# Kernel optimization log

Hardware: AMD Instinct MI355X
Metric: run time of the kernel (lower is better)

The kernel has to match this reference:

```python
import jax, jax.numpy as jnp
import numpy as np

B, S, D, H, DFF = 4, 2048, 1024, 16, 4096
HD = D // H


def setup_inputs() -> dict:
    key = jax.random.key(0)
    ks = jax.random.split(key, 12)
    sc = 0.02
    return {
        "x": jax.random.normal(ks[0], (B, S, D), jnp.float32),
        "wq": jax.random.normal(ks[1], (HD, HD), jnp.float32) * sc,
        "bq": jnp.zeros((HD,), jnp.float32),
        "wk": jax.random.normal(ks[2], (HD, HD), jnp.float32) * sc,
        "bk": jnp.zeros((HD,), jnp.float32),
        "wv": jax.random.normal(ks[3], (HD, HD), jnp.float32) * sc,
        "bv": jnp.zeros((HD,), jnp.float32),
        "wo": jax.random.normal(ks[4], (D, D), jnp.float32) * sc,
        "bo": jnp.zeros((D,), jnp.float32),
        "ln1_w": jnp.ones((D,), jnp.float32),
        "ln1_b": jnp.zeros((D,), jnp.float32),
        "w1": jax.random.normal(ks[5], (D, DFF), jnp.float32) * sc,
        "b1": jnp.zeros((DFF,), jnp.float32),
        "w2": jax.random.normal(ks[6], (DFF, D), jnp.float32) * sc,
        "b2": jnp.zeros((D,), jnp.float32),
        "ln2_w": jnp.ones((D,), jnp.float32),
        "ln2_b": jnp.zeros((D,), jnp.float32),
    }


def _layernorm(x, w, b, eps=1e-5):
    m = jnp.mean(x, axis=-1, keepdims=True)
    v = jnp.mean((x - m) ** 2, axis=-1, keepdims=True)
    return (x - m) / jnp.sqrt(v + eps) * w + b


def reference(x, wq, bq, wk, bk, wv, bv, wo, bo, ln1_w, ln1_b, w1, b1, w2, b2, ln2_w, ln2_b):
    bs, s, d = x.shape
    h = H
    hd = d // h
    # split heads: [b, h, s, hd]
    xh = x.reshape(bs, s, h, hd).transpose(0, 2, 1, 3)
    q = xh @ wq + bq  # per-head-dim linear, shared across heads (as in source)
    k = xh @ wk + bk
    v = xh @ wv + bv
    scores = jnp.einsum("bhqd,bhkd->bhqk", q, k) / (hd ** 0.5)
    # faithful quirk: tril then mask-where-zero -> -inf
    tri = jnp.tril(scores)
    masked = jnp.where(tri == 0, -jnp.inf, tri)
    attn = jax.nn.softmax(masked, axis=-1)
    o = attn @ v  # [b, h, s, hd]
    o = o.transpose(0, 2, 1, 3).reshape(bs, s, d)
    o = o @ wo + bo
    x = _layernorm(x + o, ln1_w, ln1_b)
    ff = jax.nn.gelu(x @ w1 + b1, approximate=False) @ w2 + b2  # dropout is identity in eval
    x = _layernorm(x + ff, ln2_w, ln2_b)
    return x
```

## Files before the change

### kernel.cpp

```cpp
#include <hip/hip_runtime.h>

typedef unsigned short u16;
typedef unsigned int u32;
typedef float f32x4 __attribute__((ext_vector_type(4)));
typedef short s16x8 __attribute__((ext_vector_type(8)));
typedef u16 u16x8 __attribute__((ext_vector_type(8)));
typedef u32 u32x4 __attribute__((ext_vector_type(4)));

#define DEV static __device__ __forceinline__

DEV u16 f2bf(float f){
  unsigned u = __float_as_uint(f);
  u += 0x7fffu + ((u>>16)&1u);
  return (u16)(u>>16);
}

DEV float bf2f(u16 h){ return __uint_as_float((u32)h << 16); }

DEV u32 cvt_pk_bf16(float lo, float hi){
  u32 r;
  asm("v_cvt_pk_bf16_f32 %0, %1, %2" : "=v"(r) : "v"(lo), "v"(hi));
  return r;
}

DEV f32x4 mfma_bf16(s16x8 a, s16x8 b, f32x4 c){
  return __builtin_amdgcn_mfma_f32_16x16x32_bf16(a, b, c, 0, 0, 0);
}

DEV void gll16(const void* g, void* l){
  __builtin_amdgcn_global_load_lds((const __attribute__((address_space(1))) u32*)g,
                                   (__attribute__((address_space(3))) u32*)l, 16, 0, 0);
}

__global__ __launch_bounds__(256) void transpose_cast(const float* __restrict__ w,
                                                      u16* __restrict__ wt,
                                                      int K, int N){
  __shared__ float tile[32][33];
  int n0 = blockIdx.x * 32, k0 = blockIdx.y * 32;
  int tx = threadIdx.x & 31, ty = threadIdx.x >> 5;
  #pragma unroll
  for(int j = 0; j < 32; j += 8)
    tile[ty + j][tx] = w[(size_t)(k0 + ty + j) * N + n0 + tx];
  __syncthreads();
  #pragma unroll
  for(int j = 0; j < 32; j += 8)
    wt[(size_t)(n0 + ty + j) * K + k0 + tx] = f2bf(tile[tx][ty + j]);
}

__global__ __launch_bounds__(256) void qkv_kernel(const float* __restrict__ x,
    const float* __restrict__ wq, const float* __restrict__ bq,
    const float* __restrict__ wk, const float* __restrict__ bk,
    const float* __restrict__ wv, const float* __restrict__ bv,
    u16* __restrict__ qo, u16* __restrict__ ko, u16* __restrict__ vo){
  __shared__ float ws[3 * 64 * 64];
  __shared__ float xs[32 * 64];
  __shared__ float vls[64 * 33];
  int h  = blockIdx.y;
  int r0 = blockIdx.x * 32;
  for(int i = threadIdx.x; i < 1024; i += 256) ((float4*)ws)[i]        = ((const float4*)wq)[i];
  for(int i = threadIdx.x; i < 1024; i += 256) ((float4*)ws)[1024 + i] = ((const float4*)wk)[i];
  for(int i = threadIdx.x; i < 1024; i += 256) ((float4*)ws)[2048 + i] = ((const float4*)wv)[i];
  for(int i = threadIdx.x; i < 512; i += 256){
    int r = i >> 4, c4 = (i & 15) * 4;
    ((float4*)xs)[i] = *(const float4*)(x + (size_t)(r0 + r) * 1024 + h * 64 + c4);
  }
  __syncthreads();
  int r  = threadIdx.x >> 3;
  int j0 = (threadIdx.x & 7) * 8;
  float aq[8], ak[8], av[8];
  #pragma unroll
  for(int j = 0; j < 8; j++){ aq[j] = 0.f; ak[j] = 0.f; av[j] = 0.f; }
  for(int i = 0; i < 64; i++){
    float xv = xs[r * 64 + i];
    const float* wr = ws + i * 64 + j0;
    #pragma unroll
    for(int j = 0; j < 8; j++){
      aq[j] = fmaf(xv, wr[j],        aq[j]);
      ak[j] = fmaf(xv, wr[4096 + j], ak[j]);
      av[j] = fmaf(xv, wr[8192 + j], av[j]);
    }
  }
  int b = r0 >> 11, s0 = r0 & 2047;
  int bh = b * 16 + h;
  size_t base = ((size_t)bh * 2048 + s0 + r) * 64 + j0;
  ushort4 q_lo = { f2bf(aq[0]+bq[j0+0]), f2bf(aq[1]+bq[j0+1]), f2bf(aq[2]+bq[j0+2]), f2bf(aq[3]+bq[j0+3]) };
  ushort4 q_hi = { f2bf(aq[4]+bq[j0+4]), f2bf(aq[5]+bq[j0+5]), f2bf(aq[6]+bq[j0+6]), f2bf(aq[7]+bq[j0+7]) };
  ushort4 k_lo = { f2bf(ak[0]+bk[j0+0]), f2bf(ak[1]+bk[j0+1]), f2bf(ak[2]+bk[j0+2]), f2bf(ak[3]+bk[j0+3]) };
  ushort4 k_hi = { f2bf(ak[4]+bk[j0+4]), f2bf(ak[5]+bk[j0+5]), f2bf(ak[6]+bk[j0+6]), f2bf(ak[7]+bk[j0+7]) };
  *(ushort4*)(qo + base)     = q_lo;  *(ushort4*)(qo + base + 4) = q_hi;
  *(ushort4*)(ko + base)     = k_lo;  *(ushort4*)(ko + base + 4) = k_hi;
  #pragma unroll
  for(int j = 0; j < 8; j++) vls[(j0 + j) * 33 + r] = av[j] + bv[j0 + j];
  __syncthreads();
  size_t vtb = (size_t)bh * 64 * 2048 + s0;
  for(int i = threadIdx.x; i < 2048; i += 256){
    int d = i >> 5, sl = i & 31;
    vo[vtb + (size_t)d * 2048 + sl] = f2bf(vls[d * 33 + sl]);
  }
}

__global__ __launch_bounds__(256, 5) void attn_kernel(const u16* __restrict__ q,
                                                      const u16* __restrict__ k,
                                                      const u16* __restrict__ vT,
                                                      u16* __restrict__ o){
  __shared__ u16 ksh[2 * 64 * 64];
  __shared__ u16 vsh[2 * 64 * 64];
  int bi = blockIdx.x;
  int bh = bi & 63;
  int qt = 31 - (bi >> 6);
  int w = threadIdx.x >> 6, lane = threadIdx.x & 63;
  int l15 = lane & 15, l4 = lane >> 4;
  size_t kvbase = (size_t)bh * 2048 * 64;
  size_t vtbase = (size_t)bh * 64 * 2048;
  int b_ = bh >> 4, h = bh & 15;
  f32x4 zero = {0.f, 0.f, 0.f, 0.f};

  int r8 = lane >> 3, c8 = lane & 7;
  int swz = ((c8 ^ r8) << 3);
  int roff = (l15 & 7) << 3;
  int rx   = l15 & 7;
  int o4   = (l4 & 1) << 2;

  s16x8 qf[2];
  #pragma unroll
  for(int kc = 0; kc < 2; kc++){
    u16x8 qr = *(const u16x8*)(q + kvbase + (size_t)(qt*64 + w*16 + l15)*64 + kc*32 + l4*8);
    union { u32x4 u; s16x8 h; } pk;
    #pragma unroll
    for(int r = 0; r < 4; r++)
      pk.u[r] = cvt_pk_bf16(bf2f(qr[2*r]) * 0.125f, bf2f(qr[2*r+1]) * 0.125f);
    qf[kc] = pk.h;
  }

  f32x4 accO[4];
  #pragma unroll
  for(int md = 0; md < 4; md++) accO[md] = zero;
  float lrow = 0.f;

  #pragma unroll
  for(int j = 0; j < 2; j++){
    int row = w*16 + j*8 + r8;
    gll16(k  + kvbase + (size_t)row*64 + swz,   ksh + row*64 + c8*8);
    gll16(vT + vtbase + (size_t)row*2048 + swz, vsh + row*64 + c8*8);
  }
  __syncthreads();

  #pragma unroll 1
  for(int kt = 0; kt <= qt; kt++){
    int cur = kt & 1;
    if(kt < qt){
      int nb = cur ^ 1, k1 = kt + 1;
      #pragma unroll
      for(int j = 0; j < 2; j++){
        int row = w*16 + j*8 + r8;
        gll16(k  + kvbase + (size_t)(k1*64 + row)*64 + swz,  ksh + nb*4096 + row*64 + c8*8);
        gll16(vT + vtbase + (size_t)row*2048 + k1*64 + swz,  vsh + nb*4096 + row*64 + c8*8);
      }
    }
    const u16* kb = ksh + cur*4096;
    const u16* vb = vsh + cur*4096;

    f32x4 sc[4];
    #pragma unroll
    for(int mk = 0; mk < 4; mk++){
      s16x8 kf0 = *(const s16x8*)(kb + (mk*16 + l15)*64 + ((l4*8) ^ roff));
      s16x8 kf1 = *(const s16x8*)(kb + (mk*16 + l15)*64 + ((32 + l4*8) ^ roff));
      f32x4 a = zero;
      a = mfma_bf16(kf0, qf[0], a);
      a = mfma_bf16(kf1, qf[1], a);
      sc[mk] = a;
    }
    if(kt == qt){
      int ql = w*16 + l15;
      #pragma unroll
      for(int mk = 0; mk < 4; mk++){
        int kl = mk*16 + l4*4;
        #pragma unroll
        for(int b = 0; b < 4; b++)
          if(kl + b > ql) sc[mk][b] = -3.0e38f;
      }
    }
    #pragma unroll
    for(int mk = 0; mk < 4; mk++)
      #pragma unroll
      for(int b = 0; b < 4; b++)
        sc[mk][b] = __expf(fminf(sc[mk][b], 8.f));
    f32x4 s4 = sc[0] + sc[1] + sc[2] + sc[3];
    lrow += (s4[0] + s4[1]) + (s4[2] + s4[3]);

    u32 plo[4], phi[4];
    #pragma unroll
    for(int mk = 0; mk < 4; mk++){
      plo[mk] = cvt_pk_bf16(sc[mk][0], sc[mk][1]);
      phi[mk] = cvt_pk_bf16(sc[mk][2], sc[mk][3]);
    }
    #pragma unroll
    for(int kc = 0; kc < 2; kc++){
      union { u32x4 u; s16x8 h; } pb;
      pb.u[0] = plo[2*kc];   pb.u[1] = phi[2*kc];
      pb.u[2] = plo[2*kc+1]; pb.u[3] = phi[2*kc+1];
      int bB = 4*kc + (l4 >> 1);
      s16x8 vf[4];
      #pragma unroll
      for(int md = 0; md < 4; md++){
        const u16* vrow = vb + (md*16 + l15)*64;
        union { struct{ uint2 a, b; } p; s16x8 h; } vv;
        vv.p.a = *(const uint2*)(vrow + (((bB    ) ^ rx) << 3) + o4);
        vv.p.b = *(const uint2*)(vrow + (((bB + 2) ^ rx) << 3) + o4);
        vf[md] = vv.h;
      }
      __builtin_amdgcn_s_setprio(1);
      #pragma unroll
      for(int md = 0; md < 4; md++)
        accO[md] = mfma_bf16(vf[md], pb.h, accO[md]);
      __builtin_amdgcn_s_setprio(0);
    }
    __syncthreads();
  }

  lrow += __shfl_xor(lrow, 16);
  lrow += __shfl_xor(lrow, 32);
  float inv = 1.f / lrow;
  int qrow = qt*64 + w*16 + l15;
  #pragma unroll
  for(int md = 0; md < 4; md++){
    int d0 = md*16 + l4*4;
    ushort4 ov;
    ov.x = f2bf(accO[md][0] * inv);
    ov.y = f2bf(accO[md][1] * inv);
    ov.z = f2bf(accO[md][2] * inv);
    ov.w = f2bf(accO[md][3] * inv);
    *(ushort4*)(o + ((size_t)(b_*2048 + qrow))*1024 + h*64 + d0) = ov;
  }
}

template<int EPI, int BM, int BN, int WM, int WN>
__global__ __launch_bounds__(WM*WN*64) void gemm_dbuf(const u16* __restrict__ A,
    const u16* __restrict__ Bt, const float* __restrict__ bias,
    const float* __restrict__ resid, float* __restrict__ Cf,
    int M, int N, int K, int ntn){
  constexpr int THREADS = WM*WN*64;
  constexpr int RM = BM/(WM*16), RN = BN/(WN*16);
  constexpr int LDSH = (BM+BN)*64;
  constexpr int RSTEP = THREADS/8;
  constexpr int PA = BM/RSTEP, PB = BN/RSTEP;
  __shared__ u16 lds[2*LDSH];

  int nwg = gridDim.x;
  int cq = nwg >> 3;
  int wg = ((int)blockIdx.x & 7) * cq + ((int)blockIdx.x >> 3);
  int tm = wg / ntn, tn = wg % ntn;

  int tid = threadIdx.x, lane = tid & 63, w = tid >> 6;
  int wm = w / WN, wn = w % WN;
  int l15 = lane & 15, l4 = lane >> 4;

  f32x4 zero = {0.f, 0.f, 0.f, 0.f};
  f32x4 acc[RM][RN];
  #pragma unroll
  for(int m = 0; m < RM; m++)
    #pragma unroll
    for(int n = 0; n < RN; n++) acc[m][n] = zero;

  int srow = tid >> 3, scol = (tid & 7) * 8;
  const u16* Ag = A  + ((size_t)tm*BM + srow)*(size_t)K + scol;
  const u16* Bg = Bt + ((size_t)tn*BN + srow)*(size_t)K + scol;
  int ldsAo = srow*64 + scol;
  int ldsBo = BM*64 + srow*64 + scol;

  int NT = K >> 6;
  #pragma unroll
  for(int p = 0; p < PA; p++) gll16(Ag + (size_t)p*RSTEP*K, lds + ldsAo + p*RSTEP*64);
  #pragma unroll
  for(int p = 0; p < PB; p++) gll16(Bg + (size_t)p*RSTEP*K, lds + ldsBo + p*RSTEP*64);
  __syncthreads();

  int wr = wm * (BM/WM), wc = wn * (BN/WN);
  for(int t = 0; t < NT; t++){
    const u16* buf = lds + (t & 1) * LDSH;
    if(t + 1 < NT){
      u16* nbuf = lds + ((t + 1) & 1) * LDSH;
      int kt = (t + 1) << 6;
      #pragma unroll
      for(int p = 0; p < PA; p++) gll16(Ag + (size_t)p*RSTEP*K + kt, nbuf + ldsAo + p*RSTEP*64);
      #pragma unroll
      for(int p = 0; p < PB; p++) gll16(Bg + (size_t)p*RSTEP*K + kt, nbuf + ldsBo + p*RSTEP*64);
    }
    #pragma unroll
    for(int kc = 0; kc < 2; kc++){
      s16x8 af[RM], bfr[RN];
      #pragma unroll
      for(int m = 0; m < RM; m++) af[m]  = *(const s16x8*)(buf + (wr + m*16 + l15)*64 + kc*32 + l4*8);
      #pragma unroll
      for(int n = 0; n < RN; n++) bfr[n] = *(const s16x8*)(buf + BM*64 + (wc + n*16 + l15)*64 + kc*32 + l4*8);
      #pragma unroll
      for(int m = 0; m < RM; m++)
        #pragma unroll
        for(int n = 0; n < RN; n++)
          acc[m][n] = mfma_bf16(af[m], bfr[n], acc[m][n]);
    }
    __syncthreads();
  }

  int row0 = tm*BM + wr, col0 = tn*BN + wc;
  #pragma unroll
  for(int n = 0; n < RN; n++){
    int col = col0 + n*16 + l15;
    float bcol = bias[col];
    #pragma unroll
    for(int m = 0; m < RM; m++){
      #pragma unroll
      for(int b4 = 0; b4 < 4; b4++){
        int row = row0 + m*16 + l4*4 + b4;
        size_t oi = (size_t)row * N + col;
        Cf[oi] = acc[m][n][b4] + bcol + resid[oi];
      }
    }
  }
}

template<int EPI, int BN, int SPLITK>
__global__ __launch_bounds__(512, 2) void gemm_8ph(const u16* __restrict__ A,
    const u16* __restrict__ Bt, const float* __restrict__ bias,
    float* __restrict__ Cf, u16* __restrict__ Cb,
    int M, int N, int LDA, int Kloop, int ntn){
  constexpr int NPP = BN / 128;
  constexpr int BLOADS = BN / 128;
  __shared__ u16 lds[32768 + 4 * BN * 32];

  auto Aoff = [](int b, int kc){ return b*16384 + kc*8192; };
  auto Boff = [](int b, int kc){ return 32768 + (b*2 + kc) * BN * 32; };

  int nwg = gridDim.x;
  int cq = nwg >> 3;
  int wg = ((int)blockIdx.x & 7) * cq + ((int)blockIdx.x >> 3);
  int ks = 0;
  if constexpr (SPLITK == 2){ ks = wg & 1; wg >>= 1; }
  int tm = wg / ntn, tn = wg % ntn;

  int tid = threadIdx.x, lane = tid & 63, w = tid >> 6;
  int wm = w >> 2, wn = w & 3;
  int l15 = lane & 15, l4 = lane >> 4;

  const u16* Ag = A  + (size_t)tm * 256 * LDA + (size_t)ks * Kloop;
  const u16* Bg = Bt + (size_t)tn * BN  * LDA + (size_t)ks * Kloop;

  f32x4 zero = {0.f, 0.f, 0.f, 0.f};
  f32x4 acc[8][2*NPP];
  #pragma unroll
  for(int m = 0; m < 8; m++)
    #pragma unroll
    for(int n = 0; n < 2*NPP; n++) acc[m][n] = zero;

  int NT = Kloop >> 6;

  auto stA = [&](int st, int skc, int sbuf){
    #pragma unroll
    for(int j = 0; j < 2; j++){
      int row = (tid >> 2) + j * 128;
      int sc = (((tid & 3) ^ ((row >> 1) & 3)) << 3);
      gll16(Ag + (size_t)row * LDA + st*64 + skc*32 + sc,
            lds + Aoff(sbuf, skc) + row*32 + (tid & 3)*8);
    }
  };
  auto stB = [&](int st, int skc, int sbuf){
    #pragma unroll
    for(int j = 0; j < BLOADS; j++){
      int row = (tid >> 2) + j * 128;
      int sc = (((tid & 3) ^ ((row >> 1) & 3)) << 3);
      gll16(Bg + (size_t)row * LDA + st*64 + skc*32 + sc,
            lds + Boff(sbuf, skc) + row*32 + (tid & 3)*8);
    }
  };

  stA(0, 0, 0); stB(0, 0, 0);
  stA(0, 1, 0); stB(0, 1, 0);
  stA(1, 0, 1); stB(1, 0, 1);
  stA(1, 1, 1);
  if constexpr (BN == 256) asm volatile("s_waitcnt vmcnt(4)" ::: "memory");
  else                     asm volatile("s_waitcnt vmcnt(3)" ::: "memory");
  __builtin_amdgcn_s_barrier();

  s16x8 af[8], bf[NPP];
  for(int it = 0; it < (NT >> 1); ++it){
    int t0 = it << 1;
    #pragma unroll
    for(int p = 0; p < 8; p++){
      const int nh = p & 1, kc = (p >> 1) & 1, bsel = p >> 2;
      if(nh == 0){
        #pragma unroll
        for(int m = 0; m < 8; m++){
          int arow = wm*128 + m*16 + l15;
          af[m] = *(const s16x8*)(lds + Aoff(bsel, kc) + arow*32 + ((l4 ^ ((arow>>1)&3)) << 3));
        }
      }
      #pragma unroll
      for(int n = 0; n < NPP; n++){
        int brow = wn*(BN/4) + nh*(BN/8) + n*16 + l15;
        bf[n] = *(const s16x8*)(lds + Boff(bsel, kc) + brow*32 + ((l4 ^ ((brow>>1)&3)) << 3));
      }
      {
        constexpr int SKC[8] = {1,0,0,1,1,0,0,1};
        constexpr int SBF[8] = {1,0,0,0,0,1,1,1};
        constexpr int TOF[8] = {1,2,2,2,2,3,3,3};
        int st = t0 + TOF[p]; if(st > NT - 1) st = NT - 1;
        if(p & 1) stA(st, SKC[p], SBF[p]);
        else      stB(st, SKC[p], SBF[p]);
      }
      __builtin_amdgcn_s_barrier();
      asm volatile("s_waitcnt lgkmcnt(0)" ::: "memory");
      __builtin_amdgcn_s_setprio(1);
      #pragma unroll
      for(int m = 0; m < 8; m++)
        #pragma unroll
        for(int n = 0; n < NPP; n++)
          acc[m][nh*NPP + n] = mfma_bf16(af[m], bf[n], acc[m][nh*NPP + n]);
      __builtin_amdgcn_s_setprio(0);
      if(p == 3 || p == 7){
        if constexpr (BN == 256) asm volatile("s_waitcnt vmcnt(4)" ::: "memory");
        else                     asm volatile("s_waitcnt vmcnt(3)" ::: "memory");
      }
      __builtin_amdgcn_s_barrier();
    }
  }

  int row0 = tm*256 + wm*128, col0 = tn*BN + wn*(BN/4);
  float* Cfp = Cf;
  if constexpr (EPI == 3) Cfp = Cf + (size_t)ks * M * N;
  #pragma unroll
  for(int nh = 0; nh < 2; nh++)
    #pragma unroll
    for(int n = 0; n < NPP; n++){
      int j = nh*NPP + n;
      int col = col0 + nh*(BN/8) + n*16 + l15;
      float bcol = 0.f;
      if constexpr (EPI == 1) bcol = bias[col];
      #pragma unroll
      for(int m = 0; m < 8; m++){
        #pragma unroll
        for(int b4 = 0; b4 < 4; b4++){
          int row = row0 + m*16 + l4*4 + b4;
          size_t oi = (size_t)row * N + col;
          if constexpr (EPI == 1){
            float vout = acc[m][j][b4] + bcol;
            float uu = 0.7978845608f * vout * (1.f + 0.044715f * vout * vout);
            float e  = __expf(2.f * uu);
            float th = 1.f - __fdividef(2.f, e + 1.f);
            Cb[oi] = f2bf(0.5f * vout * (1.f + th));
          } else {
            Cfp[oi] = acc[m][j][b4];
          }
        }
      }
    }
}

__global__ __launch_bounds__(256) void ln_kernel(const float* __restrict__ a,
                                                 const float* __restrict__ w,
                                                 const float* __restrict__ bvec,
                                                 u16* __restrict__ outb){
  int row = blockIdx.x;
  float4 val = ((const float4*)(a + (size_t)row * 1024))[threadIdx.x];
  float s  = val.x + val.y + val.z + val.w;
  float ss = val.x * val.x + val.y * val.y + val.z * val.z + val.w * val.w;
  #pragma unroll
  for(int off = 32; off > 0; off >>= 1){
    s  += __shfl_down(s, off);
    ss += __shfl_down(ss, off);
  }
  __shared__ float sb[8];
  int lane = threadIdx.x & 63, wv = threadIdx.x >> 6;
  if(lane == 0){ sb[wv] = s; sb[4 + wv] = ss; }
  __syncthreads();
  s  = sb[0] + sb[1] + sb[2] + sb[3];
  ss = sb[4] + sb[5] + sb[6] + sb[7];
  float mean = s * (1.f / 1024.f);
  float var  = ss * (1.f / 1024.f) - mean * mean;
  float rstd = rsqrtf(var + 1e-5f);
  int c = threadIdx.x * 4;
  float4 w4 = *(const float4*)(w + c);
  float4 b4 = *(const float4*)(bvec + c);
  ushort4 ob;
  ob.x = f2bf((val.x - mean) * rstd * w4.x + b4.x);
  ob.y = f2bf((val.y - mean) * rstd * w4.y + b4.y);
  ob.z = f2bf((val.z - mean) * rstd * w4.z + b4.z);
  ob.w = f2bf((val.w - mean) * rstd * w4.w + b4.w);
  *(ushort4*)(outb + (size_t)row * 1024 + c) = ob;
}

__global__ __launch_bounds__(256) void ln2_kernel(const float* __restrict__ p0,
                                                  const float* __restrict__ p1,
                                                  const u16* __restrict__ residb,
                                                  const float* __restrict__ b2,
                                                  const float* __restrict__ w,
                                                  const float* __restrict__ bvec,
                                                  float* __restrict__ outf){
  int row = blockIdx.x;
  int c = threadIdx.x * 4;
  float4 v0 = ((const float4*)(p0 + (size_t)row * 1024))[threadIdx.x];
  float4 v1 = ((const float4*)(p1 + (size_t)row * 1024))[threadIdx.x];
  ushort4 rb = *(const ushort4*)(residb + (size_t)row * 1024 + c);
  float4 bb = *(const float4*)(b2 + c);
  float4 val;
  val.x = v0.x + v1.x + bb.x + bf2f(rb.x);
  val.y = v0.y + v1.y + bb.y + bf2f(rb.y);
  val.z = v0.z + v1.z + bb.z + bf2f(rb.z);
  val.w = v0.w + v1.w + bb.w + bf2f(rb.w);
  float s  = val.x + val.y + val.z + val.w;
  float ss = val.x * val.x + val.y * val.y + val.z * val.z + val.w * val.w;
  #pragma unroll
  for(int off = 32; off > 0; off >>= 1){
    s  += __shfl_down(s, off);
    ss += __shfl_down(ss, off);
  }
  __shared__ float sb[8];
  int lane = threadIdx.x & 63, wv = threadIdx.x >> 6;
  if(lane == 0){ sb[wv] = s; sb[4 + wv] = ss; }
  __syncthreads();
  s  = sb[0] + sb[1] + sb[2] + sb[3];
  ss = sb[4] + sb[5] + sb[6] + sb[7];
  float mean = s * (1.f / 1024.f);
  float var  = ss * (1.f / 1024.f) - mean * mean;
  float rstd = rsqrtf(var + 1e-5f);
  float4 w4 = *(const float4*)(w + c);
  float4 b4 = *(const float4*)(bvec + c);
  float4 o4v;
  o4v.x = (val.x - mean) * rstd * w4.x + b4.x;
  o4v.y = (val.y - mean) * rstd * w4.y + b4.y;
  o4v.z = (val.z - mean) * rstd * w4.z + b4.z;
  o4v.w = (val.w - mean) * rstd * w4.w + b4.w;
  ((float4*)(outf + (size_t)row * 1024))[threadIdx.x] = o4v;
}

extern "C" void kernel_launch(void* const* d_in, const int* in_sizes, int n_in,
                              void* d_out, int out_size, void* d_ws, size_t ws_size,
                              hipStream_t stream){
  const float* x    = (const float*)d_in[0];
  const float* wq   = (const float*)d_in[1];
  const float* bq   = (const float*)d_in[2];
  const float* wk   = (const float*)d_in[3];
  const float* bk   = (const float*)d_in[4];
  const float* wv   = (const float*)d_in[5];
  const float* bv   = (const float*)d_in[6];
  const float* wo   = (const float*)d_in[7];
  const float* bo   = (const float*)d_in[8];
  const float* ln1w = (const float*)d_in[9];
  const float* ln1b = (const float*)d_in[10];
  const float* w1   = (const float*)d_in[11];
  const float* b1   = (const float*)d_in[12];
  const float* w2   = (const float*)d_in[13];
  const float* b2   = (const float*)d_in[14];
  const float* ln2w = (const float*)d_in[15];
  const float* ln2b = (const float*)d_in[16];
  float* out = (float*)d_out;

  char* ws8 = (char*)d_ws;
  u16*   qb  = (u16*)  (ws8 + ((size_t)0   << 20));
  u16*   kb  = (u16*)  (ws8 + ((size_t)16  << 20));
  u16*   vb  = (u16*)  (ws8 + ((size_t)32  << 20));
  u16*   ob  = (u16*)  (ws8 + ((size_t)48  << 20));
  u16*   wot = (u16*)  (ws8 + ((size_t)64  << 20));
  u16*   w1t = (u16*)  (ws8 + ((size_t)66  << 20));
  u16*   w2t = (u16*)  (ws8 + ((size_t)74  << 20));
  u16*   tb  = (u16*)  (ws8 + ((size_t)82  << 20));
  u16*   gb  = (u16*)  (ws8 + ((size_t)98  << 20));
  float* rr  = (float*)(ws8 + ((size_t)162 << 20));

  transpose_cast<<<dim3(32, 32),  256, 0, stream>>>(wo, wot, 1024, 1024);
  transpose_cast<<<dim3(128, 32), 256, 0, stream>>>(w1, w1t, 1024, 4096);
  transpose_cast<<<dim3(32, 128), 256, 0, stream>>>(w2, w2t, 4096, 1024);

  qkv_kernel<<<dim3(256, 16), 256, 0, stream>>>(x, wq, bq, wk, bk, wv, bv, qb, kb, vb);
  attn_kernel<<<dim3(2048), 256, 0, stream>>>(qb, kb, vb, ob);

  gemm_dbuf<0,128,128,2,2><<<dim3(512), 256, 0, stream>>>(ob, wot, bo, x, rr, 8192, 1024, 1024, 8);
  ln_kernel<<<dim3(8192), 256, 0, stream>>>(rr, ln1w, ln1b, tb);
  gemm_8ph<1,256,1><<<dim3(512), 512, 0, stream>>>(tb, w1t, b1, nullptr, gb, 8192, 4096, 1024, 1024, 16);
  gemm_8ph<3,256,2><<<dim3(256), 512, 0, stream>>>(gb, w2t, nullptr, rr, nullptr, 8192, 1024, 4096, 2048, 4);
  ln2_kernel<<<dim3(8192), 256, 0, stream>>>(rr, rr + (size_t)8192*1024, tb, b2, ln2w, ln2b, out);
}
```

Baseline: 385.5 us.

## Process two N-tiles per workgroup in FFN1 GEMM and store split-K partials as bf16

The FFN1 GEMM now has each workgroup compute two adjacent 256-wide N tiles in sequence, reusing the A tile's address setup. The next tile's prologue loads are issued before the epilogue of the current one, and the grid is halved to 256 workgroups. The split-K FFN2 GEMM now writes its partial sums as bf16 instead of fp32, and ln2 reads them as bf16, which halves the partial-sum traffic. Fewer workgroups means less parallelism per CU wave, and rounding the partials to bf16 reduces accuracy.

```diff
diff --git a/kernel.cpp b/kernel.cpp
--- a/kernel.cpp
+++ b/kernel.cpp
@@ -319,7 +319,7 @@
   }
 }
 
-template<int EPI, int BN, int SPLITK>
+template<int EPI, int BN, int SPLITK, int PAIR>
 __global__ __launch_bounds__(512, 2) void gemm_8ph(const u16* __restrict__ A,
     const u16* __restrict__ Bt, const float* __restrict__ bias,
     float* __restrict__ Cf, u16* __restrict__ Cb,
@@ -336,21 +336,13 @@
   int wg = ((int)blockIdx.x & 7) * cq + ((int)blockIdx.x >> 3);
   int ks = 0;
   if constexpr (SPLITK == 2){ ks = wg & 1; wg >>= 1; }
-  int tm = wg / ntn, tn = wg % ntn;
+  int tm = wg / ntn, tnp = wg % ntn;
 
   int tid = threadIdx.x, lane = tid & 63, w = tid >> 6;
   int wm = w >> 2, wn = w & 3;
   int l15 = lane & 15, l4 = lane >> 4;
 
-  const u16* Ag = A  + (size_t)tm * 256 * LDA + (size_t)ks * Kloop;
-  const u16* Bg = Bt + (size_t)tn * BN  * LDA + (size_t)ks * Kloop;
-
-  f32x4 zero = {0.f, 0.f, 0.f, 0.f};
-  f32x4 acc[8][2*NPP];
-  #pragma unroll
-  for(int m = 0; m < 8; m++)
-    #pragma unroll
-    for(int n = 0; n < 2*NPP; n++) acc[m][n] = zero;
+  const u16* Ag = A + (size_t)tm * 256 * LDA + (size_t)ks * Kloop;
 
   int NT = Kloop >> 6;
 
@@ -363,7 +355,7 @@
             lds + Aoff(sbuf, skc) + row*32 + (tid & 3)*8);
     }
   };
-  auto stB = [&](int st, int skc, int sbuf){
+  auto stB = [&](const u16* Bg, int st, int skc, int sbuf){
     #pragma unroll
     for(int j = 0; j < BLOADS; j++){
       int row = (tid >> 2) + j * 128;
@@ -372,87 +364,115 @@
             lds + Boff(sbuf, skc) + row*32 + (tid & 3)*8);
     }
   };
-
-  stA(0, 0, 0); stB(0, 0, 0);
-  stA(0, 1, 0); stB(0, 1, 0);
-  stA(1, 0, 1); stB(1, 0, 1);
-  stA(1, 1, 1);
-  if constexpr (BN == 256) asm volatile("s_waitcnt vmcnt(4)" ::: "memory");
-  else                     asm volatile("s_waitcnt vmcnt(3)" ::: "memory");
-  __builtin_amdgcn_s_barrier();
-
+  auto prologue = [&](const u16* Bg){
+    stA(0, 0, 0); stB(Bg, 0, 0, 0);
+    stA(0, 1, 0); stB(Bg, 0, 1, 0);
+    stA(1, 0, 1); stB(Bg, 1, 0, 1);
+    stA(1, 1, 1);
+  };
+
+  f32x4 zero = {0.f, 0.f, 0.f, 0.f};
+  f32x4 acc[8][2*NPP];
   s16x8 af[8], bf[NPP];
-  for(int it = 0; it < (NT >> 1); ++it){
-    int t0 = it << 1;
-    #pragma unroll
-    for(int p = 0; p < 8; p++){
-      const int nh = p & 1, kc = (p >> 1) & 1, bsel = p >> 2;
-      if(nh == 0){
+
+  #pragma unroll
+  for(int sub = 0; sub < PAIR; ++sub){
+    int tn = tnp * PAIR + sub;
+    const u16* Bg = Bt + (size_t)tn * BN * LDA + (size_t)ks * Kloop;
+    #pragma unroll
+    for(int m = 0; m < 8; m++)
+      #pragma unroll
+      for(int n = 0; n < 2*NPP; n++) acc[m][n] = zero;
+
+    if(sub == 0){
+      prologue(Bg);
+      if constexpr (BN == 256) asm volatile("s_waitcnt vmcnt(4)" ::: "memory");
+      else                     asm volatile("s_waitcnt vmcnt(3)" ::: "memory");
+      __builtin_amdgcn_s_barrier();
+    }
+
+    for(int it = 0; it < (NT >> 1); ++it){
+      int t0 = it << 1;
+      #pragma unroll
+      for(int p = 0; p < 8; p++){
+        const int nh = p & 1, kc = (p >> 1) & 1, bsel = p >> 2;
+        if(nh == 0){
+          #pragma unroll
+          for(int m = 0; m < 8; m++){
+            int arow = wm*128 + m*16 + l15;
+            af[m] = *(const s16x8*)(lds + Aoff(bsel, kc) + arow*32 + ((l4 ^ ((arow>>1)&3)) << 3));
+          }
+        }
+        #pragma unroll
+        for(int n = 0; n < NPP; n++){
+          int brow = wn*(BN/4) + nh*(BN/8) + n*16 + l15;
+          bf[n] = *(const s16x8*)(lds + Boff(bsel, kc) + brow*32 + ((l4 ^ ((brow>>1)&3)) << 3));
+        }
+        {
+          constexpr int SKC[8] = {1,0,0,1,1,0,0,1};
+          constexpr int SBF[8] = {1,0,0,0,0,1,1,1};
+          constexpr int TOF[8] = {1,2,2,2,2,3,3,3};
+          int st = t0 + TOF[p]; if(st > NT - 1) st = NT - 1;
+          if(p & 1) stA(st, SKC[p], SBF[p]);
+          else      stB(Bg, st, SKC[p], SBF[p]);
+        }
+        __builtin_amdgcn_s_barrier();
+        asm volatile("s_waitcnt lgkmcnt(0)" ::: "memory");
+        __builtin_amdgcn_s_setprio(1);
+        #pragma unroll
+        for(int m = 0; m < 8; m++)
+          #pragma unroll
+          for(int n = 0; n < NPP; n++)
+            acc[m][nh*NPP + n] = mfma_bf16(af[m], bf[n], acc[m][nh*NPP + n]);
+        __builtin_amdgcn_s_setprio(0);
+        if(p == 3 || p == 7){
+          if constexpr (BN == 256) asm volatile("s_waitcnt vmcnt(4)" ::: "memory");
+          else                     asm volatile("s_waitcnt vmcnt(3)" ::: "memory");
+        }
+        __builtin_amdgcn_s_barrier();
+      }
+    }
+
+    if(sub + 1 < PAIR){
+      asm volatile("s_waitcnt vmcnt(0)" ::: "memory");
+      const u16* Bg2 = Bt + (size_t)(tn + 1) * BN * LDA + (size_t)ks * Kloop;
+      prologue(Bg2);
+    }
+
+    int row0 = tm*256 + wm*128, col0 = tn*BN + wn*(BN/4);
+    #pragma unroll
+    for(int nh = 0; nh < 2; nh++)
+      #pragma unroll
+      for(int n = 0; n < NPP; n++){
+        int j = nh*NPP + n;
+        int col = col0 + nh*(BN/8) + n*16 + l15;
+        float bcol = 0.f;
+        if constexpr (EPI == 1) bcol = bias[col];
         #pragma unroll
         for(int m = 0; m < 8; m++){
-          int arow = wm*128 + m*16 + l15;
-          af[m] = *(const s16x8*)(lds + Aoff(bsel, kc) + arow*32 + ((l4 ^ ((arow>>1)&3)) << 3));
-        }
-      }
-      #pragma unroll
-      for(int n = 0; n < NPP; n++){
-        int brow = wn*(BN/4) + nh*(BN/8) + n*16 + l15;
-        bf[n] = *(const s16x8*)(lds + Boff(bsel, kc) + brow*32 + ((l4 ^ ((brow>>1)&3)) << 3));
-      }
-      {
-        constexpr int SKC[8] = {1,0,0,1,1,0,0,1};
-        constexpr int SBF[8] = {1,0,0,0,0,1,1,1};
-        constexpr int TOF[8] = {1,2,2,2,2,3,3,3};
-        int st = t0 + TOF[p]; if(st > NT - 1) st = NT - 1;
-        if(p & 1) stA(st, SKC[p], SBF[p]);
-        else      stB(st, SKC[p], SBF[p]);
-      }
-      __builtin_amdgcn_s_barrier();
-      asm volatile("s_waitcnt lgkmcnt(0)" ::: "memory");
-      __builtin_amdgcn_s_setprio(1);
-      #pragma unroll
-      for(int m = 0; m < 8; m++)
-        #pragma unroll
-        for(int n = 0; n < NPP; n++)
-          acc[m][nh*NPP + n] = mfma_bf16(af[m], bf[n], acc[m][nh*NPP + n]);
-      __builtin_amdgcn_s_setprio(0);
-      if(p == 3 || p == 7){
-        if constexpr (BN == 256) asm volatile("s_waitcnt vmcnt(4)" ::: "memory");
-        else                     asm volatile("s_waitcnt vmcnt(3)" ::: "memory");
-      }
-      __builtin_amdgcn_s_barrier();
-    }
-  }
-
-  int row0 = tm*256 + wm*128, col0 = tn*BN + wn*(BN/4);
-  float* Cfp = Cf;
-  if constexpr (EPI == 3) Cfp = Cf + (size_t)ks * M * N;
-  #pragma unroll
-  for(int nh = 0; nh < 2; nh++)
-    #pragma unroll
-    for(int n = 0; n < NPP; n++){
-      int j = nh*NPP + n;
-      int col = col0 + nh*(BN/8) + n*16 + l15;
-      float bcol = 0.f;
-      if constexpr (EPI == 1) bcol = bias[col];
-      #pragma unroll
-      for(int m = 0; m < 8; m++){
-        #pragma unroll
-        for(int b4 = 0; b4 < 4; b4++){
-          int row = row0 + m*16 + l4*4 + b4;
-          size_t oi = (size_t)row * N + col;
-          if constexpr (EPI == 1){
-            float vout = acc[m][j][b4] + bcol;
-            float uu = 0.7978845608f * vout * (1.f + 0.044715f * vout * vout);
-            float e  = __expf(2.f * uu);
-            float th = 1.f - __fdividef(2.f, e + 1.f);
-            Cb[oi] = f2bf(0.5f * vout * (1.f + th));
-          } else {
-            Cfp[oi] = acc[m][j][b4];
+          #pragma unroll
+          for(int b4 = 0; b4 < 4; b4++){
+            int row = row0 + m*16 + l4*4 + b4;
+            size_t oi = (size_t)row * N + col;
+            if constexpr (EPI == 1){
+              float vout = acc[m][j][b4] + bcol;
+              float uu = 0.7978845608f * vout * (1.f + 0.044715f * vout * vout);
+              float e  = __expf(2.f * uu);
+              float th = 1.f - __fdividef(2.f, e + 1.f);
+              Cb[oi] = f2bf(0.5f * vout * (1.f + th));
+            } else {
+              Cb[(size_t)ks * M * N + oi] = f2bf(acc[m][j][b4]);
+            }
           }
         }
       }
-    }
+
+    if(sub + 1 < PAIR){
+      if constexpr (BN == 256) asm volatile("s_waitcnt vmcnt(4)" ::: "memory");
+      else                     asm volatile("s_waitcnt vmcnt(3)" ::: "memory");
+      __builtin_amdgcn_s_barrier();
+    }
+  }
 }
 
 __global__ __launch_bounds__(256) void ln_kernel(const float* __restrict__ a,
@@ -488,8 +508,8 @@
   *(ushort4*)(outb + (size_t)row * 1024 + c) = ob;
 }
 
-__global__ __launch_bounds__(256) void ln2_kernel(const float* __restrict__ p0,
-                                                  const float* __restrict__ p1,
+__global__ __launch_bounds__(256) void ln2_kernel(const u16* __restrict__ p0,
+                                                  const u16* __restrict__ p1,
                                                   const u16* __restrict__ residb,
                                                   const float* __restrict__ b2,
                                                   const float* __restrict__ w,
@@ -497,15 +517,15 @@
                                                   float* __restrict__ outf){
   int row = blockIdx.x;
   int c = threadIdx.x * 4;
-  float4 v0 = ((const float4*)(p0 + (size_t)row * 1024))[threadIdx.x];
-  float4 v1 = ((const float4*)(p1 + (size_t)row * 1024))[threadIdx.x];
+  ushort4 v0 = *(const ushort4*)(p0 + (size_t)row * 1024 + c);
+  ushort4 v1 = *(const ushort4*)(p1 + (size_t)row * 1024 + c);
   ushort4 rb = *(const ushort4*)(residb + (size_t)row * 1024 + c);
   float4 bb = *(const float4*)(b2 + c);
   float4 val;
-  val.x = v0.x + v1.x + bb.x + bf2f(rb.x);
-  val.y = v0.y + v1.y + bb.y + bf2f(rb.y);
-  val.z = v0.z + v1.z + bb.z + bf2f(rb.z);
-  val.w = v0.w + v1.w + bb.w + bf2f(rb.w);
+  val.x = bf2f(v0.x) + bf2f(v1.x) + bb.x + bf2f(rb.x);
+  val.y = bf2f(v0.y) + bf2f(v1.y) + bb.y + bf2f(rb.y);
+  val.z = bf2f(v0.z) + bf2f(v1.z) + bb.z + bf2f(rb.z);
+  val.w = bf2f(v0.w) + bf2f(v1.w) + bb.w + bf2f(rb.w);
   float s  = val.x + val.y + val.z + val.w;
   float ss = val.x * val.x + val.y * val.y + val.z * val.z + val.w * val.w;
   #pragma unroll
@@ -565,6 +585,7 @@
   u16*   tb  = (u16*)  (ws8 + ((size_t)82  << 20));
   u16*   gb  = (u16*)  (ws8 + ((size_t)98  << 20));
   float* rr  = (float*)(ws8 + ((size_t)162 << 20));
+  u16*   pp  = (u16*)  (ws8 + ((size_t)162 << 20));
 
   transpose_cast<<<dim3(32, 32),  256, 0, stream>>>(wo, wot, 1024, 1024);
   transpose_cast<<<dim3(128, 32), 256, 0, stream>>>(w1, w1t, 1024, 4096);
@@ -575,7 +596,7 @@
 
   gemm_dbuf<0,128,128,2,2><<<dim3(512), 256, 0, stream>>>(ob, wot, bo, x, rr, 8192, 1024, 1024, 8);
   ln_kernel<<<dim3(8192), 256, 0, stream>>>(rr, ln1w, ln1b, tb);
-  gemm_8ph<1,256,1><<<dim3(512), 512, 0, stream>>>(tb, w1t, b1, nullptr, gb, 8192, 4096, 1024, 1024, 16);
-  gemm_8ph<3,256,2><<<dim3(256), 512, 0, stream>>>(gb, w2t, nullptr, rr, nullptr, 8192, 1024, 4096, 2048, 4);
-  ln2_kernel<<<dim3(8192), 256, 0, stream>>>(rr, rr + (size_t)8192*1024, tb, b2, ln2w, ln2b, out);
-}
+  gemm_8ph<1,256,1,2><<<dim3(256), 512, 0, stream>>>(tb, w1t, b1, nullptr, gb, 8192, 4096, 1024, 1024, 8);
+  gemm_8ph<3,256,2,1><<<dim3(256), 512, 0, stream>>>(gb, w2t, nullptr, nullptr, pp, 8192, 1024, 4096, 2048, 4);
+  ln2_kernel<<<dim3(8192), 256, 0, stream>>>(pp, pp + (size_t)8192*1024, tb, b2, ln2w, ln2b, out);
+}
```

After: 385.3 us. About the same (-0.1%).
